# Kernel tuning notes

Hardware: AMD Instinct MI355X
Metric: run time of the kernel (lower is better)

## Reference

```python
import jax, jax.numpy as jnp
import numpy as np

GAMMA = 0.3        # LinearSpike surrogate-gradient slope
TIMESTEPS = 10

@jax.custom_vjp
def linear_spike(x):
    # forward: Heaviside; backward: piecewise-linear surrogate (Bellec et al. 2018)
    return (x > 0).astype(x.dtype)

def _ls_fwd(x):
    return linear_spike(x), x

def _ls_bwd(x, g):
    return (g * GAMMA * jnp.maximum(1.0 - jnp.abs(x), 0.0),)

linear_spike.defvjp(_ls_fwd, _ls_bwd)


def setup_inputs() -> dict:
    key = jax.random.key(0)
    ks = jax.random.split(key, 6)
    V, E, H, S, B = 32000, 1024, 1024, 64, 64
    return {
        "input_batch": jax.random.randint(ks[0], (S, B), 0, V),  # [seq_len, batch]
        "embedding": jax.random.normal(ks[1], (V, E), jnp.float32),
        "W1": jax.random.normal(ks[2], (H, E), jnp.float32) / np.sqrt(E).astype(np.float32),
        "b1": jnp.zeros((H,), jnp.float32),
        "W2": jax.random.normal(ks[3], (H, H), jnp.float32) / np.sqrt(H).astype(np.float32),
        "b2": jnp.zeros((H,), jnp.float32),
        "threshold": jnp.float32(1.0),
        "leak": jnp.float32(0.95),
    }


def reference(input_batch, embedding, W1, b1, W2, b2, threshold, leak):
    # Dropout masks are identity in the deterministic reference (eval mode).
    S, B = input_batch.shape
    H = W1.shape[0]
    embed = embedding[input_batch]                       # [S, B, E]
    # First Linear is constant across timesteps of a word -> hoist out of the T loop.
    h1 = jnp.einsum('sbe,he->sbh', embed, W1) + b1       # [S, B, H]

    def word_step(carry, x):                             # x: [B, H]
        def t_step(c, _):
            mem1, mem2 = c
            # LIF dynamics
            mem1 = leak * mem1 + x
            mem_thr = mem1 / threshold - 1.0
            spike = linear_spike(mem_thr)                # surrogate-grad spike
            fired = jax.lax.stop_gradient((mem_thr > 0).astype(mem1.dtype))
            mem1 = mem1 - threshold * fired              # soft reset
            # second Linear + Integrate neuron
            mem2 = mem2 + spike @ W2.T + b2
            return (mem1, mem2), None
        carry, _ = jax.lax.scan(t_step, carry, None, length=TIMESTEPS)
        return carry, None

    init = (jnp.zeros((B, H), embed.dtype), jnp.zeros((B, H), embed.dtype))
    (mem1, mem2), _ = jax.lax.scan(word_step, init, h1)
    return mem2 / B                                      # out / embed.shape[1]
```

## Files before the change

### kernel.cpp

```cpp
#include <hip/hip_runtime.h>


#define TSTEPS 10
#define SEQ    64
#define BATCH  64
#define EDIM   1024
#define HDIM   1024
#define NROW   (SEQ * BATCH)
#define KSPLIT 16

typedef unsigned short u16;
typedef __attribute__((ext_vector_type(8))) _Float16 half8;
typedef __attribute__((ext_vector_type(8))) unsigned short ushort8;
typedef __attribute__((ext_vector_type(4))) unsigned short ushort4v;
typedef __attribute__((ext_vector_type(4))) float  f32x4;

union h16 { _Float16 f; u16 u; };

__device__ __forceinline__ u16 f2h_bits(float x) {
    h16 t; t.f = (_Float16)x; return t.u;
}
__device__ __forceinline__ float h2f(u16 b) {
    h16 t; t.u = b; return (float)t.f;
}
__device__ __forceinline__ void gld16(const u16* g, u16* l) {
    __builtin_amdgcn_global_load_lds(
        (const __attribute__((address_space(1))) void*)g,
        (__attribute__((address_space(3))) void*)l, 16, 0, 0);
}

__global__ __launch_bounds__(256) void split_pack(
    const float* __restrict__ emb, const float* __restrict__ W1,
    const int* __restrict__ idx,
    u16* __restrict__ ahi, u16* __restrict__ whi)
{
    const int t = blockIdx.x * 256 + threadIdx.x;
    const int r = t >> 7;
    const int c = (t & 127) << 3;
    if (r < NROW) {
        const int srow = idx[(r & 63) * 64 + (r >> 6)];
        const float* src = emb + (size_t)srow * EDIM + c;
        float4 v0 = *(const float4*)src;
        float4 v1 = *(const float4*)(src + 4);
        float x[8] = {v0.x, v0.y, v0.z, v0.w, v1.x, v1.y, v1.z, v1.w};
        ushort8 h;
#pragma unroll
        for (int j = 0; j < 8; ++j) h[j] = f2h_bits(x[j]);
        *(ushort8*)(ahi + (size_t)r * EDIM + c) = h;
    } else {
        const int rw = r - NROW;
        const float* src = W1 + (size_t)rw * EDIM + c;
        float4 v0 = *(const float4*)src;
        float4 v1 = *(const float4*)(src + 4);
        float x[8] = {v0.x, v0.y, v0.z, v0.w, v1.x, v1.y, v1.z, v1.w};
        ushort8 h;
#pragma unroll
        for (int j = 0; j < 8; ++j) h[j] = f2h_bits(x[j]);
        *(ushort8*)(whi + (size_t)rw * EDIM + c) = h;
    }
}

#define BM 64
#define BN 128
#define BK 32
#define NT (EDIM / BK)
#define AH 0
#define WH 2048
#define BUF 6144

__global__ __launch_bounds__(256, 3) void gemm1_h1(
    const u16* __restrict__ Ahi,
    const u16* __restrict__ Whi,
    u16* __restrict__ h1H)
{
    __shared__ float smf[9216];
    u16* stage = (u16*)smf;

    const int bid = blockIdx.x;
    const int loc = bid >> 3;
    const int by  = (bid & 7) * 8 + (loc & 7);
    const int bx  = loc >> 3;
    const int row0 = by * BM, col0 = bx * BN;

    const int tid  = threadIdx.x;
    const int wave = tid >> 6, lane = tid & 63;
    const int wn   = wave;
    const int lrow = lane & 15, kgrp = lane >> 4;

    const int srr = lane >> 2;
    const int kcs = (((lane & 3) ^ ((lane >> 3) & 3)) << 3);
    const size_t aoff = (size_t)(row0 + wave * 16 + srr) * EDIM + kcs;
    const size_t w0   = (size_t)(col0 + wave * 32 + srr) * EDIM + kcs;
    const size_t w1   = w0 + (size_t)16 * EDIM;

    f32x4 acc[4][2];
    const f32x4 zero = {0.f, 0.f, 0.f, 0.f};
#pragma unroll
    for (int m = 0; m < 4; ++m)
#pragma unroll
        for (int n = 0; n < 2; ++n) acc[m][n] = zero;

    auto STAGE = [&](int k0, int b) {
        u16* lb = stage + b * BUF;
        gld16(Ahi + aoff + k0, lb + AH + wave * 512);
        gld16(Whi + w0 + k0, lb + WH + wave * 1024);
        gld16(Whi + w1 + k0, lb + WH + wave * 1024 + 512);
    };

    auto COMPUTE = [&](int b) {
        const u16* lb = stage + b * BUF;
        half8 ah[4], bh[2];
#pragma unroll
        for (int n = 0; n < 2; ++n) {
            const int c = wn * 32 + n * 16 + lrow;
            const int s = kgrp ^ ((c >> 1) & 3);
            bh[n] = *(const half8*)(lb + WH + c * 32 + s * 8);
        }
#pragma unroll
        for (int m = 0; m < 4; ++m) {
            const int r = m * 16 + lrow;
            const int s = kgrp ^ ((r >> 1) & 3);
            ah[m] = *(const half8*)(lb + AH + r * 32 + s * 8);
        }
#pragma unroll
        for (int m = 0; m < 4; ++m)
#pragma unroll
            for (int n = 0; n < 2; ++n)
                acc[m][n] = __builtin_amdgcn_mfma_f32_16x16x32_f16(ah[m], bh[n], acc[m][n], 0, 0, 0);
    };

    STAGE(0, 0);
    STAGE(BK, 1);
    int cc = 0, cs = 2;
    for (int t = 0; t < NT - 2; ++t) {
        STAGE((t + 2) * BK, cs);
        asm volatile("s_waitcnt vmcnt(6)" ::: "memory");
        __builtin_amdgcn_s_barrier();
        __builtin_amdgcn_sched_barrier(0);
        COMPUTE(cc);
        __builtin_amdgcn_s_barrier();
        cc = (cc == 2) ? 0 : cc + 1;
        cs = (cs == 2) ? 0 : cs + 1;
    }
    asm volatile("s_waitcnt vmcnt(3)" ::: "memory");
    __builtin_amdgcn_s_barrier();
    __builtin_amdgcn_sched_barrier(0);
    COMPUTE(cc);
    cc = (cc == 2) ? 0 : cc + 1;
    asm volatile("s_waitcnt vmcnt(0)" ::: "memory");
    __builtin_amdgcn_s_barrier();
    __builtin_amdgcn_sched_barrier(0);
    COMPUTE(cc);

#pragma unroll
    for (int n = 0; n < 2; ++n) {
        const int col = col0 + wn * 32 + n * 16 + lrow;
        u16* base = h1H + ((size_t)by * HDIM + col) * 64 + kgrp * 4;
#pragma unroll
        for (int m = 0; m < 4; ++m) {
            ushort4v v;
#pragma unroll
            for (int j = 0; j < 4; ++j) v[j] = f2h_bits(acc[m][n][j]);
            *(ushort4v*)(base + m * 16) = v;
        }
    }
}

__global__ __launch_bounds__(256) void lif_count(
    const u16* __restrict__ h1H,
    const float* __restrict__ bias1,
    const float* __restrict__ pthr, const float* __restrict__ pleak,
    float* __restrict__ cnt)
{
    __shared__ float sm[4][64];
    const int tid  = threadIdx.x;
    const int q    = tid >> 6;
    const int lane = tid & 63;
    const int neuron = blockIdx.x * 64 + lane;
    const float thr = pthr[0];
    const float lk  = pleak[0];
    const float b1v = bias1[neuron & (HDIM - 1)];
    const u16* row = h1H + (size_t)neuron * 64;

    float mem = 0.f, c = 0.f;
    const int w0 = q * 16;
    if (q > 0) {
        ushort8 v = *(const ushort8*)(row + w0 - 8);
#pragma unroll
        for (int u = 0; u < 8; ++u) {
            const float x = h2f(v[u]) + b1v;
#pragma unroll
            for (int t = 0; t < TSTEPS; ++t) {
                mem = lk * mem + x;
                if (mem > thr) mem -= thr;
            }
        }
    }
#pragma unroll
    for (int g = 0; g < 2; ++g) {
        ushort8 v = *(const ushort8*)(row + w0 + g * 8);
#pragma unroll
        for (int u = 0; u < 8; ++u) {
            const float x = h2f(v[u]) + b1v;
#pragma unroll
            for (int t = 0; t < TSTEPS; ++t) {
                mem = lk * mem + x;
                if (mem > thr) { c += 1.f; mem -= thr; }
            }
        }
    }
    sm[q][lane] = c;
    __syncthreads();
    if (tid < 64)
        cnt[(size_t)blockIdx.x * 64 + tid] =
            sm[0][tid] + sm[1][tid] + sm[2][tid] + sm[3][tid];
}

__global__ __launch_bounds__(256) void gemm2_partial(
    const float* __restrict__ cnt,
    const float* __restrict__ W2,
    float* __restrict__ part)
{
    __shared__ float As[32][68];
    __shared__ float Bs[32][68];

    const int tid   = threadIdx.x;
    const int col0  = blockIdx.x * 64;
    const int kc    = blockIdx.y;
    const int kbase = kc * 64;

    const int lr = tid >> 3;
    const int lc = (tid & 7) * 4;
    const int tm = (tid >> 4) * 4;
    const int tn = (tid & 15) * 4;

    float acc[4][4];
#pragma unroll
    for (int i = 0; i < 4; ++i)
#pragma unroll
        for (int j = 0; j < 4; ++j) acc[i][j] = 0.f;

    for (int kt = 0; kt < 2; ++kt) {
        const int k0 = kbase + kt * 32;
#pragma unroll
        for (int p = 0; p < 2; ++p) {
            int r = p * 32 + lr;
            float4 v = *(const float4*)(cnt + (size_t)r * HDIM + k0 + lc);
            As[lc + 0][r] = v.x; As[lc + 1][r] = v.y;
            As[lc + 2][r] = v.z; As[lc + 3][r] = v.w;
        }
#pragma unroll
        for (int p = 0; p < 2; ++p) {
            int r = p * 32 + lr;
            float4 v = *(const float4*)(W2 + (size_t)(col0 + r) * HDIM + k0 + lc);
            Bs[lc + 0][r] = v.x; Bs[lc + 1][r] = v.y;
            Bs[lc + 2][r] = v.z; Bs[lc + 3][r] = v.w;
        }
        __syncthreads();
#pragma unroll 8
        for (int k = 0; k < 32; ++k) {
            float4 a  = *(const float4*)&As[k][tm];
            float4 bb = *(const float4*)&Bs[k][tn];
            float av[4] = {a.x, a.y, a.z, a.w};
            float bv[4] = {bb.x, bb.y, bb.z, bb.w};
#pragma unroll
            for (int i = 0; i < 4; ++i)
#pragma unroll
                for (int j = 0; j < 4; ++j)
                    acc[i][j] += av[i] * bv[j];
        }
        __syncthreads();
    }

#pragma unroll
    for (int i = 0; i < 4; ++i) {
        float* prow = part + (size_t)kc * (BATCH * HDIM) + (size_t)(tm + i) * HDIM + col0;
        float4 o;
        o.x = acc[i][0]; o.y = acc[i][1]; o.z = acc[i][2]; o.w = acc[i][3];
        *(float4*)(prow + tn) = o;
    }
}

__global__ __launch_bounds__(256) void reduce_out(
    const float* __restrict__ part,
    const float* __restrict__ b2,
    float* __restrict__ out)
{
    const int i = blockIdx.x * 256 + threadIdx.x;
    float s = 0.f;
#pragma unroll
    for (int kc = 0; kc < KSPLIT; ++kc)
        s += part[(size_t)kc * (BATCH * HDIM) + i];
    const int h = i & (HDIM - 1);
    out[i] = (s + (float)(SEQ * TSTEPS) * b2[h]) * (1.0f / (float)BATCH);
}

extern "C" void kernel_launch(void* const* d_in, const int* in_sizes, int n_in,
                              void* d_out, int out_size, void* d_ws, size_t ws_size,
                              hipStream_t stream)
{
    (void)in_sizes; (void)n_in; (void)out_size; (void)ws_size;

    const int*   idx  = (const int*)d_in[0];
    const float* emb  = (const float*)d_in[1];
    const float* W1   = (const float*)d_in[2];
    const float* b1   = (const float*)d_in[3];
    const float* W2   = (const float*)d_in[4];
    const float* b2   = (const float*)d_in[5];
    const float* thr  = (const float*)d_in[6];
    const float* leak = (const float*)d_in[7];
    float* out = (float*)d_out;

    char* ws = (char*)d_ws;
    float* part = (float*)ws;
    float* cnt  = (float*)(ws + (size_t)KSPLIT * BATCH * HDIM * 4);
    u16*   h1H  = (u16*)(cnt + (size_t)BATCH * HDIM);
    u16* ahi = h1H + (size_t)NROW * HDIM;
    u16* whi = ahi + (size_t)NROW * EDIM;

    split_pack<<<dim3((NROW + HDIM) * 128 / 256), 256, 0, stream>>>(
        emb, W1, idx, ahi, whi);

    gemm1_h1<<<dim3((NROW / BM) * (HDIM / BN)), 256, 0, stream>>>(
        ahi, whi, h1H);

    lif_count<<<dim3(BATCH * HDIM / 64), 256, 0, stream>>>(
        h1H, b1, thr, leak, cnt);

    gemm2_partial<<<dim3(HDIM / 64, KSPLIT), 256, 0, stream>>>(cnt, W2, part);

    reduce_out<<<dim3((BATCH * HDIM) / 256), 256, 0, stream>>>(part, b2, out);
}
```

Before: 45.34 us.

## Use 4-stage LDS ring in gemm1 and fold split-K reduction into atomics

```diff
diff --git a/kernel.cpp b/kernel.cpp
--- a/kernel.cpp
+++ b/kernel.cpp
@@ -73,7 +73,7 @@
     const u16* __restrict__ Whi,
     u16* __restrict__ h1H)
 {
-    __shared__ float smf[9216];
+    __shared__ float smf[12288];
     u16* stage = (u16*)smf;
 
     const int bid = blockIdx.x;
@@ -131,26 +131,22 @@
 
     STAGE(0, 0);
     STAGE(BK, 1);
-    int cc = 0, cs = 2;
+#pragma unroll 2
     for (int t = 0; t < NT - 2; ++t) {
-        STAGE((t + 2) * BK, cs);
+        STAGE((t + 2) * BK, (t + 2) & 3);
         asm volatile("s_waitcnt vmcnt(6)" ::: "memory");
         __builtin_amdgcn_s_barrier();
         __builtin_amdgcn_sched_barrier(0);
-        COMPUTE(cc);
-        __builtin_amdgcn_s_barrier();
-        cc = (cc == 2) ? 0 : cc + 1;
-        cs = (cs == 2) ? 0 : cs + 1;
+        COMPUTE(t & 3);
     }
     asm volatile("s_waitcnt vmcnt(3)" ::: "memory");
     __builtin_amdgcn_s_barrier();
     __builtin_amdgcn_sched_barrier(0);
-    COMPUTE(cc);
-    cc = (cc == 2) ? 0 : cc + 1;
+    COMPUTE((NT - 2) & 3);
     asm volatile("s_waitcnt vmcnt(0)" ::: "memory");
     __builtin_amdgcn_s_barrier();
     __builtin_amdgcn_sched_barrier(0);
-    COMPUTE(cc);
+    COMPUTE((NT - 1) & 3);
 
 #pragma unroll
     for (int n = 0; n < 2; ++n) {
@@ -170,10 +166,15 @@
     const u16* __restrict__ h1H,
     const float* __restrict__ bias1,
     const float* __restrict__ pthr, const float* __restrict__ pleak,
-    float* __restrict__ cnt)
+    const float* __restrict__ b2,
+    float* __restrict__ cnt, float* __restrict__ out)
 {
     __shared__ float sm[4][64];
     const int tid  = threadIdx.x;
+    const int g    = blockIdx.x * 256 + tid;
+    if (g < BATCH * HDIM)
+        out[g] = (float)(SEQ * TSTEPS) * b2[g & (HDIM - 1)] * (1.0f / (float)BATCH);
+
     const int q    = tid >> 6;
     const int lane = tid & 63;
     const int neuron = blockIdx.x * 64 + lane;
@@ -197,8 +198,8 @@
         }
     }
 #pragma unroll
-    for (int g = 0; g < 2; ++g) {
-        ushort8 v = *(const ushort8*)(row + w0 + g * 8);
+    for (int gq = 0; gq < 2; ++gq) {
+        ushort8 v = *(const ushort8*)(row + w0 + gq * 8);
 #pragma unroll
         for (int u = 0; u < 8; ++u) {
             const float x = h2f(v[u]) + b1v;
@@ -219,7 +220,7 @@
 __global__ __launch_bounds__(256) void gemm2_partial(
     const float* __restrict__ cnt,
     const float* __restrict__ W2,
-    float* __restrict__ part)
+    float* __restrict__ out)
 {
     __shared__ float As[32][68];
     __shared__ float Bs[32][68];
@@ -274,25 +275,11 @@
 
 #pragma unroll
     for (int i = 0; i < 4; ++i) {
-        float* prow = part + (size_t)kc * (BATCH * HDIM) + (size_t)(tm + i) * HDIM + col0;
-        float4 o;
-        o.x = acc[i][0]; o.y = acc[i][1]; o.z = acc[i][2]; o.w = acc[i][3];
-        *(float4*)(prow + tn) = o;
-    }
-}
-
-__global__ __launch_bounds__(256) void reduce_out(
-    const float* __restrict__ part,
-    const float* __restrict__ b2,
-    float* __restrict__ out)
-{
-    const int i = blockIdx.x * 256 + threadIdx.x;
-    float s = 0.f;
-#pragma unroll
-    for (int kc = 0; kc < KSPLIT; ++kc)
-        s += part[(size_t)kc * (BATCH * HDIM) + i];
-    const int h = i & (HDIM - 1);
-    out[i] = (s + (float)(SEQ * TSTEPS) * b2[h]) * (1.0f / (float)BATCH);
+        float* orow = out + (size_t)(tm + i) * HDIM + col0 + tn;
+#pragma unroll
+        for (int j = 0; j < 4; ++j)
+            atomicAdd(orow + j, acc[i][j] * (1.0f / (float)BATCH));
+    }
 }
 
 extern "C" void kernel_launch(void* const* d_in, const int* in_sizes, int n_in,
@@ -312,9 +299,8 @@
     float* out = (float*)d_out;
 
     char* ws = (char*)d_ws;
-    float* part = (float*)ws;
-    float* cnt  = (float*)(ws + (size_t)KSPLIT * BATCH * HDIM * 4);
-    u16*   h1H  = (u16*)(cnt + (size_t)BATCH * HDIM);
+    float* cnt = (float*)ws;
+    u16*   h1H = (u16*)(cnt + (size_t)BATCH * HDIM);
     u16* ahi = h1H + (size_t)NROW * HDIM;
     u16* whi = ahi + (size_t)NROW * EDIM;
 
@@ -325,9 +311,7 @@
         ahi, whi, h1H);
 
     lif_count<<<dim3(BATCH * HDIM / 64), 256, 0, stream>>>(
-        h1H, b1, thr, leak, cnt);
-
-    gemm2_partial<<<dim3(HDIM / 64, KSPLIT), 256, 0, stream>>>(cnt, W2, part);
-
-    reduce_out<<<dim3((BATCH * HDIM) / 256), 256, 0, stream>>>(part, b2, out);
-}
+        h1H, b1, thr, leak, b2, cnt, out);
+
+    gemm2_partial<<<dim3(HDIM / 64, KSPLIT), 256, 0, stream>>>(cnt, W2, out);
+}
```

Measured after the change: 64.39 us. +42.0%, slower.
